# Kernel optimization log

Hardware: AMD Instinct MI355X
Metric: run time of the kernel (lower is better)

The kernel has to match this reference:

```python
import jax, jax.numpy as jnp
import numpy as np

V, MAXLEN, D, FF, H, L = 50257, 1024, 768, 3072, 12, 12
HD = D // H


def _ln(x, w, b, eps=1e-5):
    mu = jnp.mean(x, axis=-1, keepdims=True)
    var = jnp.var(x, axis=-1, keepdims=True)
    return (x - mu) * jax.lax.rsqrt(var + eps) * w + b


def setup_inputs() -> dict:
    key = jax.random.key(0)
    ks = jax.random.split(key, 16)
    s = 0.02
    inp = {
        "tokens": jax.random.randint(ks[0], (2, 1024), 0, V),
        "tok_embed": jax.random.normal(ks[1], (V, D), jnp.float32) * s,
        "pos_embed": jax.random.normal(ks[2], (MAXLEN, D), jnp.float32) * s,
        # stacked per-layer params, weights stored [in, out]
        "qkv_w": jax.random.normal(ks[3], (L, D, 3 * D), jnp.float32) * s,
        "qkv_b": jnp.zeros((L, 3 * D), jnp.float32),
        "proj_w": jax.random.normal(ks[4], (L, D, D), jnp.float32) * s,
        "proj_b": jnp.zeros((L, D), jnp.float32),
        "ln1_w": jnp.ones((L, D), jnp.float32),
        "ln1_b": jnp.zeros((L, D), jnp.float32),
        "ln2_w": jnp.ones((L, D), jnp.float32),
        "ln2_b": jnp.zeros((L, D), jnp.float32),
        "fc1_w": jax.random.normal(ks[5], (L, D, FF), jnp.float32) * s,
        "fc1_b": jnp.zeros((L, FF), jnp.float32),
        "fc2_w": jax.random.normal(ks[6], (L, FF, D), jnp.float32) * s,
        "fc2_b": jnp.zeros((L, D), jnp.float32),
        "lnf_w": jnp.ones((D,), jnp.float32),
        "lnf_b": jnp.zeros((D,), jnp.float32),
    }
    return inp


def _gpt2(tokens, tok_embed, pos_embed, qkv_w, qkv_b, proj_w, proj_b,
          ln1_w, ln1_b, ln2_w, ln2_b, fc1_w, fc1_b, fc2_w, fc2_b, lnf_w, lnf_b):
    B, T = tokens.shape
    x = tok_embed[tokens] + pos_embed[jnp.arange(T)][None, :, :]  # [B,T,D]
    causal = jnp.tril(jnp.ones((T, T), bool))[None, None]          # [1,1,T,T]
    neg = jnp.finfo(x.dtype).min

    def block(x, p):
        (qw, qb, pw, pb, l1w, l1b, l2w, l2b, f1w, f1b, f2w, f2b) = p
        h = _ln(x, l1w, l1b)
        qkv = h @ qw + qb                                          # [B,T,3D]
        q, k, v = jnp.split(qkv, 3, axis=-1)
        q = q.reshape(B, T, H, HD).transpose(0, 2, 1, 3)           # [B,H,T,HD]
        k = k.reshape(B, T, H, HD).transpose(0, 2, 1, 3)
        v = v.reshape(B, T, H, HD).transpose(0, 2, 1, 3)
        att = jnp.einsum('bhqd,bhkd->bhqk', q, k) / np.sqrt(HD).astype(x.dtype)
        att = jnp.where(causal, att, neg)
        att = jax.nn.softmax(att, axis=-1)
        o = jnp.einsum('bhqk,bhkd->bhqd', att, v)
        o = o.transpose(0, 2, 1, 3).reshape(B, T, D)
        x = x + o @ pw + pb
        h2 = _ln(x, l2w, l2b)
        ff = jax.nn.gelu(h2 @ f1w + f1b, approximate=True) @ f2w + f2b
        return x + ff, None

    params = (qkv_w, qkv_b, proj_w, proj_b, ln1_w, ln1_b, ln2_w, ln2_b,
              fc1_w, fc1_b, fc2_w, fc2_b)
    x, _ = jax.lax.scan(block, x, params)
    x = _ln(x, lnf_w, lnf_b)
    return x @ tok_embed.T                                         # tied lm_head [B,T,V]


def reference(tokens, tok_embed, pos_embed, qkv_w, qkv_b, proj_w, proj_b,
              ln1_w, ln1_b, ln2_w, ln2_b, fc1_w, fc1_b, fc2_w, fc2_b,
              lnf_w, lnf_b):
    return _gpt2(tokens, tok_embed, pos_embed, qkv_w, qkv_b, proj_w, proj_b,
                 ln1_w, ln1_b, ln2_w, ln2_b, fc1_w, fc1_b, fc2_w, fc2_b,
                 lnf_w, lnf_b)
```

## Files before the change

kernel.cpp:

```cpp
#include <hip/hip_runtime.h>

#define TT 1024
#define DD 768
#define FFD 3072
#define NH 12
#define NL 12
#define HDIM 64
#define VOC 50257
#define BT 2048

typedef __attribute__((ext_vector_type(8))) __bf16 bf16x8;
typedef __attribute__((ext_vector_type(4))) float f32x4;
typedef __attribute__((ext_vector_type(4))) unsigned short u16x4;
typedef unsigned short u16;

static __device__ __forceinline__ u16 f2bf(float f) {
  unsigned int u = __float_as_uint(f);
  u += 0x7FFF + ((u >> 16) & 1);
  return (u16)(u >> 16);
}

static __device__ __forceinline__ void load_lds16(const u16* g, u16* l) {
  __builtin_amdgcn_global_load_lds(
      (const __attribute__((address_space(1))) unsigned int*)g,
      (__attribute__((address_space(3))) unsigned int*)l, 16, 0, 0);
}

__global__ __launch_bounds__(256) void transpose_convert(
    const float* __restrict__ in, u16* __restrict__ out, int R, int C) {
  __shared__ float tile[32][33];
  const long long zo = (long long)blockIdx.z * R * C;
  const int c0 = blockIdx.x * 32, r0 = blockIdx.y * 32;
  const int tx = threadIdx.x & 31, ty = threadIdx.x >> 5;
#pragma unroll
  for (int i = 0; i < 32; i += 8)
    tile[ty + i][tx] = in[zo + (long long)(r0 + ty + i) * C + c0 + tx];
  __syncthreads();
#pragma unroll
  for (int i = 0; i < 32; i += 8)
    out[zo + (long long)(c0 + ty + i) * R + r0 + tx] = f2bf(tile[tx][ty + i]);
}

__global__ void convert_bf16(const float* __restrict__ in, u16* __restrict__ out,
                             long long n) {
  long long i = (long long)blockIdx.x * 256 + threadIdx.x;
  const long long stride = (long long)gridDim.x * 256;
  for (; i < n; i += stride) out[i] = f2bf(in[i]);
}

__global__ __launch_bounds__(256) void embed_kernel(
    const int* __restrict__ tokens, const float* __restrict__ tokE,
    const float* __restrict__ posE, float* __restrict__ x) {
  const int row = blockIdx.x;
  const int t = row & (TT - 1);
  const int tok = tokens[row];
  const int tid = threadIdx.x;
#pragma unroll
  for (int c = 0; c < 3; ++c) {
    int d = tid + c * 256;
    x[(long long)row * DD + d] = tokE[(long long)tok * DD + d] + posE[(long long)t * DD + d];
  }
}

__global__ __launch_bounds__(256) void ln_sum(
    float* __restrict__ x, const float* __restrict__ pp, int nsum,
    const float* __restrict__ w, const float* __restrict__ b,
    u16* __restrict__ out) {
  const int row = blockIdx.x;
  const long long base = (long long)row * DD;
  const int tid = threadIdx.x;
  float v[3];
  float s = 0.f, s2 = 0.f;
#pragma unroll
  for (int c = 0; c < 3; ++c) {
    const int d = tid + c * 256;
    float t = x[base + d];
    for (int q = 0; q < nsum; ++q) t += pp[(long long)q * BT * DD + base + d];
    if (nsum) x[base + d] = t;
    v[c] = t; s += t; s2 += t * t;
  }
  for (int off = 32; off; off >>= 1) {
    s += __shfl_down(s, off, 64);
    s2 += __shfl_down(s2, off, 64);
  }
  __shared__ float rs[8];
  if ((tid & 63) == 0) { rs[tid >> 6] = s; rs[4 + (tid >> 6)] = s2; }
  __syncthreads();
  s = rs[0] + rs[1] + rs[2] + rs[3];
  s2 = rs[4] + rs[5] + rs[6] + rs[7];
  const float mu = s * (1.0f / DD);
  const float var = s2 * (1.0f / DD) - mu * mu;
  const float inv = rsqrtf(var + 1e-5f);
  u16* o = out + base;
#pragma unroll
  for (int c = 0; c < 3; ++c) {
    int d = tid + c * 256;
    o[d] = f2bf((v[c] - mu) * inv * w[d] + b[d]);
  }
}

__global__ __launch_bounds__(256, 3) void flash_attn(
    const u16* __restrict__ qkv, const u16* __restrict__ vT,
    u16* __restrict__ attn) {
  __shared__ __align__(16) u16 Qs[64 * 64];
  __shared__ __align__(16) u16 Ks0[64 * 64];
  __shared__ __align__(16) u16 Ks1[64 * 64];
  __shared__ __align__(16) u16 Vs0[64 * 64];
  __shared__ __align__(16) u16 Vs1[64 * 64];
  __shared__ __align__(16) u16 Ps[4 * 16 * 72];

  const int id = blockIdx.x;
  const int qt = 15 - id / 24;
  const int z = id % 24;
  const int b = z / NH, h = z - (z / NH) * NH;
  const int q0 = qt * 64;

  const int tid = threadIdx.x;
  const int lane = tid & 63;
  const int wave = __builtin_amdgcn_readfirstlane(tid >> 6);
  const int mf = lane & 15;
  const int quad = lane >> 4;

  const int srow = wave * 16 + (lane >> 3);
  const int srow1 = srow + 8;
  const int sch0 = (((lane & 7) ^ ((srow >> 1) & 7))) * 8;
  const int sch1 = (((lane & 7) ^ ((srow1 >> 1) & 7))) * 8;
  const int lb = wave * 1024;

  const u16* qk_base = qkv + (long long)b * TT * 2304 + h * 64;

  auto stageKV = [&](u16* Kd, u16* Vd, int kv0) {
    load_lds16(qk_base + (long long)(kv0 + srow) * 2304 + 768 + sch0, Kd + lb);
    load_lds16(qk_base + (long long)(kv0 + srow1) * 2304 + 768 + sch1, Kd + lb + 512);
    load_lds16(vT + (long long)(z * 64 + srow) * 1024 + kv0 + sch0, Vd + lb);
    load_lds16(vT + (long long)(z * 64 + srow1) * 1024 + kv0 + sch1, Vd + lb + 512);
  };

  load_lds16(qk_base + (long long)(q0 + srow) * 2304 + sch0, Qs + lb);
  load_lds16(qk_base + (long long)(q0 + srow1) * 2304 + sch1, Qs + lb + 512);
  stageKV(Ks0, Vs0, 0);
  __syncthreads();

  bf16x8 qfr[2];
  {
    const int r = wave * 16 + mf;
    const int sw = (r >> 1) & 7;
#pragma unroll
    for (int ks = 0; ks < 2; ++ks)
      qfr[ks] = *(const bf16x8*)(Qs + r * 64 + (((ks * 4 + quad) ^ sw) * 8));
  }

  f32x4 oacc[4] = {};
  float mrun = -1e30f, lrun = 0.f;
  u16 *Kc = Ks0, *Vc = Vs0, *Kn = Ks1, *Vn = Vs1;

  for (int t = 0; t <= qt; ++t) {
    if (t < qt) stageKV(Kn, Vn, (t + 1) * 64);
    const int diag = (t == qt);

    f32x4 sacc[4] = {};
#pragma unroll
    for (int ks = 0; ks < 2; ++ks)
#pragma unroll
      for (int i = 0; i < 4; ++i) {
        const int r = i * 16 + mf;
        bf16x8 kfr = *(const bf16x8*)(Kc + r * 64 + (((ks * 4 + quad) ^ ((r >> 1) & 7)) * 8));
        sacc[i] = __builtin_amdgcn_mfma_f32_16x16x32_bf16(kfr, qfr[ks], sacc[i], 0, 0, 0);
      }

    float pv[4][4];
    float tmax = -1e30f;
#pragma unroll
    for (int i = 0; i < 4; ++i)
#pragma unroll
      for (int r = 0; r < 4; ++r) {
        float v = sacc[i][r] * 0.125f;
        if (diag) {
          const int kvl = i * 16 + quad * 4 + r;
          if (kvl > wave * 16 + mf) v = -1e30f;
        }
        pv[i][r] = v;
        tmax = fmaxf(tmax, v);
      }
    tmax = fmaxf(tmax, __shfl_xor(tmax, 16, 64));
    tmax = fmaxf(tmax, __shfl_xor(tmax, 32, 64));
    const float mnew = fmaxf(mrun, tmax);
    const float fac = __expf(mrun - mnew);
    float lsum = 0.f;
#pragma unroll
    for (int i = 0; i < 4; ++i)
#pragma unroll
      for (int r = 0; r < 4; ++r) {
        float e = __expf(pv[i][r] - mnew);
        pv[i][r] = e;
        lsum += e;
      }
    lsum += __shfl_xor(lsum, 16, 64);
    lsum += __shfl_xor(lsum, 32, 64);
    lrun = lrun * fac + lsum;
    mrun = mnew;

    float fo[4];
#pragma unroll
    for (int r = 0; r < 4; ++r) fo[r] = __shfl(fac, (lane & 48) | (quad * 4 + r), 64);
#pragma unroll
    for (int j = 0; j < 4; ++j)
#pragma unroll
      for (int r = 0; r < 4; ++r) oacc[j][r] *= fo[r];

#pragma unroll
    for (int i = 0; i < 4; ++i) {
      u16x4 pk;
#pragma unroll
      for (int r = 0; r < 4; ++r) pk[r] = f2bf(pv[i][r]);
      *(u16x4*)(Ps + wave * 1152 + mf * 72 + i * 16 + quad * 4) = pk;
    }
#pragma unroll
    for (int ks = 0; ks < 2; ++ks) {
      bf16x8 pfr = *(const bf16x8*)(Ps + wave * 1152 + mf * 72 + ks * 32 + quad * 8);
#pragma unroll
      for (int j = 0; j < 4; ++j) {
        const int r = j * 16 + mf;
        bf16x8 vfr = *(const bf16x8*)(Vc + r * 64 + (((ks * 4 + quad) ^ ((r >> 1) & 7)) * 8));
        oacc[j] = __builtin_amdgcn_mfma_f32_16x16x32_bf16(pfr, vfr, oacc[j], 0, 0, 0);
      }
    }
    __syncthreads();
    u16* tk = Kc; Kc = Kn; Kn = tk;
    u16* tv = Vc; Vc = Vn; Vn = tv;
  }

  const float linv = 1.0f / lrun;
  float li[4];
#pragma unroll
  for (int r = 0; r < 4; ++r) li[r] = __shfl(linv, (lane & 48) | (quad * 4 + r), 64);
#pragma unroll
  for (int j = 0; j < 4; ++j)
#pragma unroll
    for (int r = 0; r < 4; ++r) {
      const int q = q0 + wave * 16 + quad * 4 + r;
      const int d = j * 16 + mf;
      attn[(long long)(b * TT + q) * 768 + h * 64 + d] = f2bf(oacc[j][r] * li[r]);
    }
}

enum { EPI_F32 = 0, EPI_BF16_BIAS = 1, EPI_BF16_BIAS_GELU = 2,
       EPI_BF16 = 4, EPI_QKV = 5, EPI_SPLITK_PART = 6 };

template <int EPI>
__global__ __launch_bounds__(256, 3) void gemm_nt(
    const u16* __restrict__ A, const u16* __restrict__ Bm,
    const float* __restrict__ bias,
    void* __restrict__ Cout, u16* __restrict__ vtAux,
    int M, int N, int K, int lda, int ldb, int ldc,
    long long aHi, long long aLo, long long bHi, long long bLo,
    long long cHi, long long cLo, int Hdiv, int swapxy,
    int xcdChunk, int kSplit) {
  __shared__ __align__(16) u16 As0[128 * 32];
  __shared__ __align__(16) u16 As1[128 * 32];
  __shared__ __align__(16) u16 Bs0[128 * 32];
  __shared__ __align__(16) u16 Bs1[128 * 32];
  const int z = blockIdx.z;
  int zb = 0, zh = 0;
  long long koff = 0;
  if (kSplit > 1) {
    const int slice = K / kSplit;
    koff = (long long)z * slice;
    K = slice;
  } else {
    zb = z / Hdiv; zh = z - zb * Hdiv;
  }
  const u16* Ab = A + zb * aHi + zh * aLo + koff;
  const u16* Bb = Bm + zb * bHi + zh * bLo + koff;
  const long long cOff = (long long)zb * cHi + (long long)zh * cLo;

  int rx = blockIdx.x, ry = blockIdx.y;
  if (xcdChunk) {
    const int id = ry * gridDim.x + rx;
    const int w = (id & 7) * xcdChunk + (id >> 3);
    rx = w % gridDim.x;
    ry = w / gridDim.x;
  }
  const int bx = swapxy ? ry : rx;
  const int by = swapxy ? rx : ry;
  const int m0 = by * 128;
  const int n0 = bx * 128;

  const int tid = threadIdx.x;
  const int lane = tid & 63;
  const int wave = __builtin_amdgcn_readfirstlane(tid >> 6);
  const int wm = (wave >> 1) * 64;
  const int wn = (wave & 1) * 64;
  const int mf = lane & 15;
  const int quad = lane >> 4;

  const int sr0 = wave * 32 + (lane >> 2);
  const int sr1 = sr0 + 16;
  const int sc0 = ((lane & 3) ^ ((sr0 >> 1) & 3)) * 8;
  const int sc1 = ((lane & 3) ^ ((sr1 >> 1) & 3)) * 8;
  int br0 = n0 + sr0; if (br0 >= N) br0 = N - 1;
  int br1 = n0 + sr1; if (br1 >= N) br1 = N - 1;
  const u16* agp0 = Ab + (long long)(m0 + sr0) * lda + sc0;
  const u16* agp1 = Ab + (long long)(m0 + sr1) * lda + sc1;
  const u16* bgp0 = Bb + (long long)br0 * ldb + sc0;
  const u16* bgp1 = Bb + (long long)br1 * ldb + sc1;
  const int woff = wave * 1024;

  auto stage = [&](u16* Ad, u16* Bd, int kk) {
    load_lds16(agp0 + kk, Ad + woff);
    load_lds16(agp1 + kk, Ad + woff + 512);
    load_lds16(bgp0 + kk, Bd + woff);
    load_lds16(bgp1 + kk, Bd + woff + 512);
  };

  int aoff[4], boff[4];
#pragma unroll
  for (int i = 0; i < 4; ++i) {
    const int ar = wm + i * 16 + mf;
    aoff[i] = ar * 32 + ((quad ^ ((ar >> 1) & 3)) * 8);
    const int br = wn + i * 16 + mf;
    boff[i] = br * 32 + ((quad ^ ((br >> 1) & 3)) * 8);
  }

  f32x4 acc[4][4] = {};

  auto compute = [&](const u16* Asb, const u16* Bsb) {
    bf16x8 afr[4], bfr[4];
#pragma unroll
    for (int i = 0; i < 4; ++i) afr[i] = *(const bf16x8*)(Asb + aoff[i]);
#pragma unroll
    for (int j = 0; j < 4; ++j) bfr[j] = *(const bf16x8*)(Bsb + boff[j]);
#pragma unroll
    for (int i = 0; i < 4; ++i)
#pragma unroll
      for (int j = 0; j < 4; ++j)
        acc[i][j] = __builtin_amdgcn_mfma_f32_16x16x32_bf16(afr[i], bfr[j], acc[i][j], 0, 0, 0);
  };

  stage(As0, Bs0, 0);
  __syncthreads();
  for (int k0 = 0; k0 < K; k0 += 64) {
    if (k0 + 32 < K) stage(As1, Bs1, k0 + 32);
    compute(As0, Bs0);
    __syncthreads();
    if (k0 + 64 < K) stage(As0, Bs0, k0 + 64);
    compute(As1, Bs1);
    __syncthreads();
  }

#pragma unroll
  for (int j = 0; j < 4; ++j) {
    const int col = n0 + wn + j * 16 + mf;
    if (col >= N) continue;
    float bv = 0.0f;
    if (EPI == EPI_BF16_BIAS || EPI == EPI_BF16_BIAS_GELU || EPI == EPI_QKV)
      bv = bias[col];
    if (EPI == EPI_SPLITK_PART && z == 0) bv = bias[col];
    if (EPI == EPI_QKV && col >= 1536) {
      const int hd = col - 1536;
#pragma unroll
      for (int i = 0; i < 4; ++i) {
        const int t0 = m0 + wm + i * 16 + quad * 4;
        u16x4 pk;
#pragma unroll
        for (int r = 0; r < 4; ++r) pk[r] = f2bf(acc[i][j][r] + bv);
        const int b_ = t0 >> 10;
        const long long vi =
            ((long long)((b_ * NH + (hd >> 6)) * 64 + (hd & 63))) * 1024 + (t0 & 1023);
        *(u16x4*)(vtAux + vi) = pk;
      }
      continue;
    }
#pragma unroll
    for (int i = 0; i < 4; ++i) {
#pragma unroll
      for (int r = 0; r < 4; ++r) {
        const int row = m0 + wm + i * 16 + quad * 4 + r;
        float v = acc[i][j][r] + bv;
        if (EPI == EPI_BF16_BIAS_GELU) {
          float u = v + 0.044715f * v * v * v;
          v = 0.5f * v * (1.0f + tanhf(0.7978845608028654f * u));
        }
        if (EPI == EPI_SPLITK_PART) {
          ((float*)Cout)[(long long)z * M * ldc + (long long)row * ldc + col] = v;
        } else {
          const long long ci = cOff + (long long)row * ldc + col;
          if (EPI == EPI_F32) {
            ((float*)Cout)[ci] = v;
          } else {
            ((u16*)Cout)[ci] = f2bf(v);
          }
        }
      }
    }
  }
}

extern "C" void kernel_launch(void* const* d_in, const int* in_sizes, int n_in,
                              void* d_out, int out_size, void* d_ws, size_t ws_size,
                              hipStream_t stream) {
  const int* tokens      = (const int*)d_in[0];
  const float* tok_embed = (const float*)d_in[1];
  const float* pos_embed = (const float*)d_in[2];
  const float* qkv_w     = (const float*)d_in[3];
  const float* qkv_b     = (const float*)d_in[4];
  const float* proj_w    = (const float*)d_in[5];
  const float* proj_b    = (const float*)d_in[6];
  const float* ln1_w     = (const float*)d_in[7];
  const float* ln1_b     = (const float*)d_in[8];
  const float* ln2_w     = (const float*)d_in[9];
  const float* ln2_b     = (const float*)d_in[10];
  const float* fc1_w     = (const float*)d_in[11];
  const float* fc1_b     = (const float*)d_in[12];
  const float* fc2_w     = (const float*)d_in[13];
  const float* fc2_b     = (const float*)d_in[14];
  const float* lnf_w     = (const float*)d_in[15];
  const float* lnf_b     = (const float*)d_in[16];

  if (ws_size < 440u * 1024u * 1024u) return;

  char* p = (char*)d_ws;
  auto alloc = [&](size_t bytes) {
    void* r = (void*)p;
    p += (bytes + 255) & ~(size_t)255;
    return r;
  };
  u16* wq   = (u16*)alloc((size_t)NL * 2304 * 768 * 2);
  u16* wp   = (u16*)alloc((size_t)NL * 768 * 768 * 2);
  u16* w1   = (u16*)alloc((size_t)NL * 3072 * 768 * 2);
  u16* w2   = (u16*)alloc((size_t)NL * 768 * 3072 * 2);
  u16* te   = (u16*)alloc((size_t)VOC * 768 * 2);
  float* x  = (float*)alloc((size_t)BT * 768 * 4);
  u16* hbuf = (u16*)alloc((size_t)BT * 768 * 2);
  u16* qkv  = (u16*)alloc((size_t)BT * 2304 * 2);
  u16* vT   = (u16*)alloc((size_t)24 * 64 * 1024 * 2);
  u16* attn = (u16*)alloc((size_t)BT * 768 * 2);
  u16* ff   = (u16*)alloc((size_t)BT * 3072 * 2);
  u16* xf   = (u16*)alloc((size_t)BT * 768 * 2);
  float* pp = (float*)alloc((size_t)4 * BT * 768 * 4);

  transpose_convert<<<dim3(2304 / 32, 768 / 32, NL), 256, 0, stream>>>(qkv_w, wq, 768, 2304);
  transpose_convert<<<dim3(768 / 32, 768 / 32, NL), 256, 0, stream>>>(proj_w, wp, 768, 768);
  transpose_convert<<<dim3(3072 / 32, 768 / 32, NL), 256, 0, stream>>>(fc1_w, w1, 768, 3072);
  transpose_convert<<<dim3(768 / 32, 3072 / 32, NL), 256, 0, stream>>>(fc2_w, w2, 3072, 768);
  convert_bf16<<<4096, 256, 0, stream>>>(tok_embed, te, (long long)VOC * 768);
  embed_kernel<<<BT, 256, 0, stream>>>(tokens, tok_embed, pos_embed, x);

  for (int l = 0; l < NL; ++l) {
    ln_sum<<<BT, 256, 0, stream>>>(x, pp, l == 0 ? 0 : 4,
                                   ln1_w + l * 768, ln1_b + l * 768, hbuf);
    gemm_nt<EPI_QKV><<<dim3(2304 / 128, BT / 128, 1), 256, 0, stream>>>(
        hbuf, wq + (size_t)l * 2304 * 768, qkv_b + l * 2304, qkv, vT,
        BT, 2304, 768, 768, 768, 2304, 0, 0, 0, 0, 0, 0, 1, 0, 288 / 8, 1);
    flash_attn<<<384, 256, 0, stream>>>(qkv, vT, attn);
    gemm_nt<EPI_SPLITK_PART><<<dim3(768 / 128, BT / 128, 3), 256, 0, stream>>>(
        attn, wp + (size_t)l * 768 * 768, proj_b + l * 768, pp, nullptr,
        BT, 768, 768, 768, 768, 768, 0, 0, 0, 0, 0, 0, 1, 0, 96 / 8, 3);
    ln_sum<<<BT, 256, 0, stream>>>(x, pp, 3,
                                   ln2_w + l * 768, ln2_b + l * 768, hbuf);
    gemm_nt<EPI_BF16_BIAS_GELU><<<dim3(3072 / 128, BT / 128, 1), 256, 0, stream>>>(
        hbuf, w1 + (size_t)l * 3072 * 768, fc1_b + l * 3072, ff, nullptr,
        BT, 3072, 768, 768, 768, 3072, 0, 0, 0, 0, 0, 0, 1, 0, 384 / 8, 1);
    gemm_nt<EPI_SPLITK_PART><<<dim3(768 / 128, BT / 128, 4), 256, 0, stream>>>(
        ff, w2 + (size_t)l * 768 * 3072, fc2_b + l * 768, pp, nullptr,
        BT, 768, 3072, 3072, 3072, 768, 0, 0, 0, 0, 0, 0, 1, 0, 96 / 8, 4);
  }
  ln_sum<<<BT, 256, 0, stream>>>(x, pp, 4, lnf_w, lnf_b, xf);
  gemm_nt<EPI_F32><<<dim3(BT / 128, (VOC + 127) / 128, 1), 256, 0, stream>>>(
      xf, te, nullptr, (float*)d_out, nullptr,
      BT, VOC, 768, 768, 768, VOC, 0, 0, 0, 0, 0, 0, 1, 1, 6288 / 8, 1);
}
```

Measured before the change: 2.504 ms.

## Add dedicated 256x256-tile LM-head GEMM kernel with swizzled block order

Replaces the generic 128x128 gemm_nt call for the tied LM-head projection with a specialized kernel using 256x256 tiles, 512 threads, double-buffered swizzled LDS staging via global_load_lds, and bf16 MFMA 16x16x32. Block IDs are remapped so that consecutive blocks share B (embedding) tiles across all 8 M-tiles, improving L2 reuse of the large vocab matrix. The bigger tile raises arithmetic intensity but increases register and LDS pressure (128 accumulator floats per thread). Out-of-range vocab rows are clamped on load and masked on store.

```diff
diff --git a/kernel.cpp b/kernel.cpp
--- a/kernel.cpp
+++ b/kernel.cpp
@@ -396,6 +396,97 @@
   }
 }
 
+__global__ __launch_bounds__(512, 2) void gemm_lmhead(
+    const u16* __restrict__ A, const u16* __restrict__ Bm,
+    float* __restrict__ C, int N) {
+  __shared__ __align__(16) u16 As[2][256 * 32];
+  __shared__ __align__(16) u16 Bs[2][256 * 32];
+
+  const int id = blockIdx.y * 8 + blockIdx.x;
+  const int w = (id & 7) * 197 + (id >> 3);
+  const int m0 = (w & 7) * 256;
+  const int n0 = (w >> 3) * 256;
+
+  const int tid = threadIdx.x;
+  const int lane = tid & 63;
+  const int wave = __builtin_amdgcn_readfirstlane(tid >> 6);
+  const int wr = wave >> 2;
+  const int wc = wave & 3;
+  const int mf = lane & 15;
+  const int quad = lane >> 4;
+
+  const int srow0 = wave * 16 + (lane >> 2);
+  const int srow1 = srow0 + 128;
+  const int sc0 = ((lane & 3) ^ ((srow0 >> 1) & 3)) * 8;
+  const int sc1 = ((lane & 3) ^ ((srow1 >> 1) & 3)) * 8;
+  const u16* agp0 = A + (long long)(m0 + srow0) * 768 + sc0;
+  const u16* agp1 = A + (long long)(m0 + srow1) * 768 + sc1;
+  int br0 = n0 + srow0; if (br0 >= N) br0 = N - 1;
+  int br1 = n0 + srow1; if (br1 >= N) br1 = N - 1;
+  const u16* bgp0 = Bm + (long long)br0 * 768 + sc0;
+  const u16* bgp1 = Bm + (long long)br1 * 768 + sc1;
+  const int woff0 = wave * 16 * 32;
+  const int woff1 = (128 + wave * 16) * 32;
+
+  auto stage = [&](int buf, int kk) {
+    load_lds16(agp0 + kk, &As[buf][woff0]);
+    load_lds16(agp1 + kk, &As[buf][woff1]);
+    load_lds16(bgp0 + kk, &Bs[buf][woff0]);
+    load_lds16(bgp1 + kk, &Bs[buf][woff1]);
+  };
+
+  int aoff[8], boff[4];
+#pragma unroll
+  for (int i = 0; i < 8; ++i) {
+    const int ar = wr * 128 + i * 16 + mf;
+    aoff[i] = ar * 32 + ((quad ^ ((ar >> 1) & 3)) * 8);
+  }
+#pragma unroll
+  for (int j = 0; j < 4; ++j) {
+    const int br = wc * 64 + j * 16 + mf;
+    boff[j] = br * 32 + ((quad ^ ((br >> 1) & 3)) * 8);
+  }
+
+  f32x4 acc[8][4] = {};
+
+  auto compute = [&](int buf) {
+    bf16x8 afr[8], bfr[4];
+#pragma unroll
+    for (int j = 0; j < 4; ++j) bfr[j] = *(const bf16x8*)(&Bs[buf][boff[j]]);
+#pragma unroll
+    for (int i = 0; i < 8; ++i) afr[i] = *(const bf16x8*)(&As[buf][aoff[i]]);
+#pragma unroll
+    for (int i = 0; i < 8; ++i)
+#pragma unroll
+      for (int j = 0; j < 4; ++j)
+        acc[i][j] = __builtin_amdgcn_mfma_f32_16x16x32_bf16(afr[i], bfr[j], acc[i][j], 0, 0, 0);
+  };
+
+  stage(0, 0);
+  __syncthreads();
+  for (int k0 = 0; k0 < 768; k0 += 64) {
+    if (k0 + 32 < 768) stage(1, k0 + 32);
+    compute(0);
+    __syncthreads();
+    if (k0 + 64 < 768) stage(0, k0 + 64);
+    compute(1);
+    __syncthreads();
+  }
+
+#pragma unroll
+  for (int j = 0; j < 4; ++j) {
+    const int col = n0 + wc * 64 + j * 16 + mf;
+    if (col >= N) continue;
+#pragma unroll
+    for (int i = 0; i < 8; ++i)
+#pragma unroll
+      for (int r = 0; r < 4; ++r) {
+        const int row = m0 + wr * 128 + i * 16 + quad * 4 + r;
+        C[(long long)row * N + col] = acc[i][j][r];
+      }
+  }
+}
+
 extern "C" void kernel_launch(void* const* d_in, const int* in_sizes, int n_in,
                               void* d_out, int out_size, void* d_ws, size_t ws_size,
                               hipStream_t stream) {
@@ -466,7 +557,5 @@
         BT, 768, 3072, 3072, 3072, 768, 0, 0, 0, 0, 0, 0, 1, 0, 96 / 8, 4);
   }
   ln_sum<<<BT, 256, 0, stream>>>(x, pp, 4, lnf_w, lnf_b, xf);
-  gemm_nt<EPI_F32><<<dim3(BT / 128, (VOC + 127) / 128, 1), 256, 0, stream>>>(
-      xf, te, nullptr, (float*)d_out, nullptr,
-      BT, VOC, 768, 768, 768, VOC, 0, 0, 0, 0, 0, 0, 1, 1, 6288 / 8, 1);
-}
+  gemm_lmhead<<<dim3(8, 197), 512, 0, stream>>>(xf, te, (float*)d_out, VOC);
+}
```

New measurement: 2.603 ms. +4.0%, slower.
